# Kernel optimization log

Measured on AMD Instinct MI355X. Metric: run time of the kernel, lower is better.

## Reference

```python
import jax, jax.numpy as jnp
import numpy as np

N_NODES = 100000   # number of graph nodes
N_EDGES = 1600000  # adjacency nnz (avg degree 16)
FEAT_NNZ = 1600000 # sparse feature nnz (~16 per node)
F_IN = 512
F_OUT = 128


def setup_inputs() -> dict:
    key = jax.random.key(0)
    k1, k2, k3, k4, k5, k6 = jax.random.split(key, 6)
    adj_indices = jax.random.randint(k1, (2, N_EDGES), 0, N_NODES, dtype=jnp.int64 if jax.config.jax_enable_x64 else jnp.int32)
    adj_values = jax.random.uniform(k2, (N_EDGES,), dtype=jnp.float32)
    feat_rows = jax.random.randint(k3, (FEAT_NNZ,), 0, N_NODES)
    feat_cols = jax.random.randint(k4, (FEAT_NNZ,), 0, F_IN)
    feat_values = jax.random.uniform(k5, (FEAT_NNZ,), dtype=jnp.float32)
    # xavier_uniform init of the dense weight, as in the torch module
    bound = float(np.sqrt(6.0 / (F_IN + F_OUT)))
    weight = jax.random.uniform(k6, (F_IN, F_OUT), dtype=jnp.float32, minval=-bound, maxval=bound)
    return {
        "adj_indices": adj_indices,
        "adj_values": adj_values,
        "feat_rows": feat_rows,
        "feat_cols": feat_cols,
        "feat_values": feat_values,
        "weight": weight,
        "num_nodes": N_NODES,
    }


def _spmm(rows, cols, vals, num_rows, dense):
    """COO sparse [num_rows, ?] @ dense [?, K] -> [num_rows, K]."""
    msgs = vals[:, None] * dense[cols]          # [nnz, K] gather + scale
    return jax.ops.segment_sum(msgs, rows, num_segments=num_rows)


def reference(adj_indices, adj_values, feat_rows, feat_cols, feat_values, weight, num_nodes):
    # spmm(features, W): sparse [N, F_in] @ [F_in, F_out]
    base_features = _spmm(feat_rows, feat_cols, feat_values, num_nodes, weight)
    # spmm(A_hat, base): sparse [N, N] @ [N, F_out]  -- neighbor aggregation
    out = _spmm(adj_indices[0], adj_indices[1], adj_values, num_nodes, base_features)
    return out
```

## Files before the change

kernel.cpp:

```cpp
#include <hip/hip_runtime.h>
#include <stdint.h>

#define N_NODES 100000
#define F_IN    512
#define F_OUT   128
#define BROWS   128
#define NBKT    ((N_NODES + BROWS - 1) / BROWS)
#define CAP     2560
#define EPB     2048
#define WPAD    136

typedef unsigned short     u16;
typedef unsigned int       u32;
typedef unsigned long long u64;
typedef long long          i64;

__device__ __forceinline__ float b2f(u16 u) {
    union { u32 i; float f; } x; x.i = ((u32)u) << 16; return x.f;
}
__device__ __forceinline__ u16 f2b(float f) {
    u32 i = __float_as_uint(f);
    return (u16)((i + 0x7fffu + ((i >> 16) & 1u)) >> 16);
}
__device__ __forceinline__ float blo(u32 u) { return __uint_as_float(u << 16); }
__device__ __forceinline__ float bhi(u32 u) { return __uint_as_float(u & 0xFFFF0000u); }
__device__ __forceinline__ int ld_idx(const void* p, int i, int w64) {
    return w64 ? (int)((const i64*)p)[i] : ((const int*)p)[i];
}
__device__ __forceinline__ u16 ld_val_bf(const void* p, int i, int f32) {
    return f32 ? f2b(((const float*)p)[i]) : ((const u16*)p)[i];
}

__device__ __forceinline__ void ld_idx4(int* r, const void* p, int g, int w64) {
    if (w64) {
        const i64* q = (const i64*)p + 4 * (size_t)g;
        longlong2 a = *(const longlong2*)q;
        longlong2 b = *(const longlong2*)(q + 2);
        r[0] = (int)a.x; r[1] = (int)a.y; r[2] = (int)b.x; r[3] = (int)b.y;
    } else {
        int4 a = *(const int4*)((const int*)p + 4 * (size_t)g);
        r[0] = a.x; r[1] = a.y; r[2] = a.z; r[3] = a.w;
    }
}
__device__ __forceinline__ void ld_val4(u32* v, const void* p, int g, int f32) {
    if (f32) {
        float4 a = *(const float4*)((const float*)p + 4 * (size_t)g);
        v[0] = f2b(a.x); v[1] = f2b(a.y); v[2] = f2b(a.z); v[3] = f2b(a.w);
    } else {
        ushort4 a = *(const ushort4*)((const u16*)p + 4 * (size_t)g);
        v[0] = a.x; v[1] = a.y; v[2] = a.z; v[3] = a.w;
    }
}

__global__ void sniff_k(const u16* __restrict__ w, const u32* __restrict__ adj,
                        const u32* __restrict__ frows, int* __restrict__ flags,
                        int* __restrict__ gcurF, int* __restrict__ gcurA) {
    int t = threadIdx.x;
    if (t < 64) {
        u32 e0 = (w[t]      >> 7) & 0xFF;
        u32 e1 = (w[64 + t] >> 7) & 0xFF;
        u64 bad = __ballot((e0 > 0x7B) || (e1 > 0x7B));
        u64 za = __ballot(adj[2 * t + 1] == 0u);
        u64 zf = __ballot(frows[2 * t + 1] == 0u);
        if (t == 0) {
            flags[0] = (bad != 0);
            flags[1] = (__popcll(za) >= 32);
            flags[2] = (__popcll(zf) >= 32);
        }
    }
    for (int i = t; i < NBKT; i += 256) { gcurF[i] = 0; gcurA[i] = 0; }
}

__global__ __launch_bounds__(512, 4) void binFA_k(
        const void* __restrict__ frows, const void* __restrict__ fcols,
        const void* __restrict__ fvals, int M, int nFb,
        const void* __restrict__ adjbase, const void* __restrict__ avals, int E,
        const int* __restrict__ flags, int* __restrict__ gcurF, int* __restrict__ gcurA,
        u32* __restrict__ fbkt, u64* __restrict__ abkt) {
    __shared__ int hist[NBKT];
    __shared__ int hbase[NBKT];
    int t = threadIdx.x;
    for (int i = t; i < NBKT; i += 512) hist[i] = 0;
    __syncthreads();
    int f32 = flags[0];
    if ((int)blockIdx.x < nFb) {
        int f64 = flags[2];
        int start = blockIdx.x * EPB;
        int end = min(start + EPB, M);
        int g = (start >> 2) + t;
        int e0 = 4 * g;
        int r[4] = {-1, -1, -1, -1};
        int c[4]; u32 v[4];
        if (e0 + 3 < end) {
            ld_idx4(r, frows, g, f64);
            ld_idx4(c, fcols, g, f64);
            ld_val4(v, fvals, g, f32);
        } else {
            #pragma unroll
            for (int j = 0; j < 4; ++j) if (e0 + j < end) {
                r[j] = ld_idx(frows, e0 + j, f64);
                c[j] = ld_idx(fcols, e0 + j, f64);
                v[j] = ld_val_bf(fvals, e0 + j, f32);
            }
        }
        #pragma unroll
        for (int j = 0; j < 4; ++j) if (r[j] >= 0) atomicAdd(&hist[r[j] >> 7], 1);
        __syncthreads();
        for (int i = t; i < NBKT; i += 512) {
            int h = hist[i];
            hbase[i] = h ? atomicAdd(&gcurF[i], h) : 0;
            hist[i] = 0;
        }
        __syncthreads();
        #pragma unroll
        for (int j = 0; j < 4; ++j) if (r[j] >= 0) {
            int b = r[j] >> 7;
            int pos = hbase[b] + atomicAdd(&hist[b], 1);
            if (pos < CAP)
                fbkt[(size_t)b * CAP + pos] = (v[j] << 16) | ((u32)(r[j] & 127) << 9) | (u32)c[j];
        }
    } else {
        int a64 = flags[1];
        const void* acols = a64 ? (const void*)((const i64*)adjbase + E)
                                : (const void*)((const int*)adjbase + E);
        int start = ((int)blockIdx.x - nFb) * EPB;
        int end = min(start + EPB, E);
        int g = (start >> 2) + t;
        int e0 = 4 * g;
        int r[4] = {-1, -1, -1, -1};
        int c[4]; u32 v[4];
        if (e0 + 3 < end) {
            ld_idx4(r, adjbase, g, a64);
            ld_idx4(c, acols, g, a64);
            ld_val4(v, avals, g, f32);
        } else {
            #pragma unroll
            for (int j = 0; j < 4; ++j) if (e0 + j < end) {
                r[j] = ld_idx(adjbase, e0 + j, a64);
                c[j] = ld_idx(acols, e0 + j, a64);
                v[j] = ld_val_bf(avals, e0 + j, f32);
            }
        }
        #pragma unroll
        for (int j = 0; j < 4; ++j) if (r[j] >= 0) atomicAdd(&hist[r[j] >> 7], 1);
        __syncthreads();
        for (int i = t; i < NBKT; i += 512) {
            int h = hist[i];
            hbase[i] = h ? atomicAdd(&gcurA[i], h) : 0;
            hist[i] = 0;
        }
        __syncthreads();
        #pragma unroll
        for (int j = 0; j < 4; ++j) if (r[j] >= 0) {
            int b = r[j] >> 7;
            int pos = hbase[b] + atomicAdd(&hist[b], 1);
            if (pos < CAP)
                abkt[(size_t)b * CAP + pos] =
                    ((u64)v[j] << 24) | ((u64)(r[j] & 127) << 17) | (u64)(u32)c[j];
        }
    }
}

__global__ __launch_bounds__(512, 1) void stage1_k(const int* __restrict__ cnt,
        const u32* __restrict__ bkts, const void* __restrict__ W,
        const int* __restrict__ flags, u16* __restrict__ base) {
    __shared__ u16 Wlds[F_IN * WPAD];
    __shared__ u32 csr[CAP];
    __shared__ int hcnt[BROWS];
    __shared__ int roff[BROWS + 1];
    __shared__ int cur[BROWS];
    int t = threadIdx.x;
    int f32 = flags[0];
    if (!f32) {
        const u16* Wb = (const u16*)W;
        for (int idx = t; idx < F_IN * 16; idx += 512) {
            int r = idx >> 4, c = idx & 15;
            uint4 q = *(const uint4*)(Wb + r * F_OUT + c * 8);
            *(uint4*)&Wlds[r * WPAD + c * 8] = q;
        }
    }
    int w = t >> 6, lane = t & 63, g16 = lane >> 4, l16 = lane & 15;
    for (int b = blockIdx.x; b < NBKT; b += gridDim.x) {
        int n = cnt[b]; if (n > CAP) n = CAP;
        const u32* ed = bkts + (size_t)b * CAP;
        if (t < BROWS) hcnt[t] = 0;
        __syncthreads();
        u32 pb[5];
        #pragma unroll
        for (int k = 0; k < 5; ++k) { int i = t + k * 512; pb[k] = (i < n) ? ed[i] : 0u; }
        #pragma unroll
        for (int k = 0; k < 5; ++k) { int i = t + k * 512; if (i < n) atomicAdd(&hcnt[(pb[k] >> 9) & 127], 1); }
        __syncthreads();
        if (t < 64) {
            int h0 = hcnt[2 * t], h1 = hcnt[2 * t + 1];
            int s = h0 + h1, v2 = s;
            #pragma unroll
            for (int off = 1; off < 64; off <<= 1) {
                int u = __shfl_up(v2, off);
                if (t >= off) v2 += u;
            }
            int excl = v2 - s;
            roff[2 * t] = excl;     roff[2 * t + 1] = excl + h0;
            cur[2 * t]  = excl;     cur[2 * t + 1]  = excl + h0;
            if (t == 63) roff[128] = v2;
        }
        __syncthreads();
        #pragma unroll
        for (int k = 0; k < 5; ++k) {
            int i = t + k * 512;
            if (i < n) {
                u32 p = pb[k];
                int pos = atomicAdd(&cur[(p >> 9) & 127], 1);
                csr[pos] = p;
            }
        }
        __syncthreads();
        #pragma unroll
        for (int set = 0; set < 4; ++set) {
            int row = set * 32 + w * 4 + g16;
            int s = roff[row], e = roff[row + 1];
            float a0 = 0.f, a1 = 0.f, a2 = 0.f, a3 = 0.f, a4 = 0.f, a5 = 0.f, a6 = 0.f, a7 = 0.f;
            if (f32) {
                const float* Wf = (const float*)W;
                for (int j0 = s; j0 < e; j0 += 4) {
                    u32 p[4]; float4 qa[4], qb[4];
                    #pragma unroll
                    for (int k = 0; k < 4; ++k) { int jk = j0 + k; p[k] = csr[jk < e ? jk : e - 1]; }
                    #pragma unroll
                    for (int k = 0; k < 4; ++k) {
                        const float* wp = Wf + (size_t)(p[k] & 0x1FF) * F_OUT + l16 * 8;
                        qa[k] = *(const float4*)wp;
                        qb[k] = *(const float4*)(wp + 4);
                    }
                    #pragma unroll
                    for (int k = 0; k < 4; ++k) {
                        float v = (j0 + k < e) ? b2f((u16)(p[k] >> 16)) : 0.f;
                        a0 += v * qa[k].x; a1 += v * qa[k].y;
                        a2 += v * qa[k].z; a3 += v * qa[k].w;
                        a4 += v * qb[k].x; a5 += v * qb[k].y;
                        a6 += v * qb[k].z; a7 += v * qb[k].w;
                    }
                }
            } else {
                for (int j0 = s; j0 < e; j0 += 4) {
                    u32 p[4]; uint4 q[4];
                    #pragma unroll
                    for (int k = 0; k < 4; ++k) { int jk = j0 + k; p[k] = csr[jk < e ? jk : e - 1]; }
                    #pragma unroll
                    for (int k = 0; k < 4; ++k)
                        q[k] = *(const uint4*)&Wlds[(p[k] & 0x1FF) * WPAD + l16 * 8];
                    #pragma unroll
                    for (int k = 0; k < 4; ++k) {
                        float v = (j0 + k < e) ? b2f((u16)(p[k] >> 16)) : 0.f;
                        a0 += v * blo(q[k].x); a1 += v * bhi(q[k].x);
                        a2 += v * blo(q[k].y); a3 += v * bhi(q[k].y);
                        a4 += v * blo(q[k].z); a5 += v * bhi(q[k].z);
                        a6 += v * blo(q[k].w); a7 += v * bhi(q[k].w);
                    }
                }
            }
            int gr = b * BROWS + row;
            if (gr < N_NODES) {
                uint4 o;
                o.x = (u32)f2b(a0) | ((u32)f2b(a1) << 16);
                o.y = (u32)f2b(a2) | ((u32)f2b(a3) << 16);
                o.z = (u32)f2b(a4) | ((u32)f2b(a5) << 16);
                o.w = (u32)f2b(a6) | ((u32)f2b(a7) << 16);
                *(uint4*)(base + (size_t)gr * F_OUT + l16 * 8) = o;
            }
        }
        __syncthreads();
    }
}

__global__ __launch_bounds__(512, 4) void stage2_k(const int* __restrict__ cnt,
        const u64* __restrict__ bkts, const u16* __restrict__ base,
        const int* __restrict__ flags, void* __restrict__ out) {
    __shared__ u64 csr[CAP];
    __shared__ int hcnt[BROWS];
    __shared__ int roff[BROWS + 1];
    __shared__ int cur[BROWS];
    int t = threadIdx.x;
    int b = blockIdx.x;
    int n = cnt[b]; if (n > CAP) n = CAP;
    const u64* ed = bkts + (size_t)b * CAP;
    if (t < BROWS) hcnt[t] = 0;
    __syncthreads();
    u64 pb[5];
    #pragma unroll
    for (int k = 0; k < 5; ++k) { int i = t + k * 512; pb[k] = (i < n) ? ed[i] : 0ull; }
    #pragma unroll
    for (int k = 0; k < 5; ++k) { int i = t + k * 512; if (i < n) atomicAdd(&hcnt[(int)((pb[k] >> 17) & 127)], 1); }
    __syncthreads();
    if (t < 64) {
        int h0 = hcnt[2 * t], h1 = hcnt[2 * t + 1];
        int s = h0 + h1, v2 = s;
        #pragma unroll
        for (int off = 1; off < 64; off <<= 1) {
            int u = __shfl_up(v2, off);
            if (t >= off) v2 += u;
        }
        int excl = v2 - s;
        roff[2 * t] = excl;     roff[2 * t + 1] = excl + h0;
        cur[2 * t]  = excl;     cur[2 * t + 1]  = excl + h0;
        if (t == 63) roff[128] = v2;
    }
    __syncthreads();
    #pragma unroll
    for (int k = 0; k < 5; ++k) {
        int i = t + k * 512;
        if (i < n) {
            u64 p = pb[k];
            int pos = atomicAdd(&cur[(int)((p >> 17) & 127)], 1);
            csr[pos] = p;
        }
    }
    __syncthreads();
    int wave = t >> 6, lane = t & 63, g16 = lane >> 4, l16 = lane & 15;
    int f32o = flags[0];
    #pragma unroll
    for (int set = 0; set < 4; ++set) {
        int row = set * 32 + wave * 4 + g16;
        int s = roff[row], e = roff[row + 1];
        float a0 = 0.f, a1 = 0.f, a2 = 0.f, a3 = 0.f, a4 = 0.f, a5 = 0.f, a6 = 0.f, a7 = 0.f;
        for (int j0 = s; j0 < e; j0 += 8) {
            u64 p[8]; uint4 q[8];
            #pragma unroll
            for (int k = 0; k < 8; ++k) { int jk = j0 + k; p[k] = csr[jk < e ? jk : e - 1]; }
            #pragma unroll
            for (int k = 0; k < 8; ++k)
                q[k] = *(const uint4*)(base + (size_t)(u32)(p[k] & 0x1FFFF) * F_OUT + l16 * 8);
            #pragma unroll
            for (int k = 0; k < 8; ++k) {
                float v = (j0 + k < e) ? b2f((u16)(p[k] >> 24)) : 0.f;
                a0 += v * blo(q[k].x); a1 += v * bhi(q[k].x);
                a2 += v * blo(q[k].y); a3 += v * bhi(q[k].y);
                a4 += v * blo(q[k].z); a5 += v * bhi(q[k].z);
                a6 += v * blo(q[k].w); a7 += v * bhi(q[k].w);
            }
        }
        int gr = b * BROWS + row;
        if (gr < N_NODES) {
            if (f32o) {
                float* op = (float*)out + (size_t)gr * F_OUT + l16 * 8;
                float4 o0, o1;
                o0.x = a0; o0.y = a1; o0.z = a2; o0.w = a3;
                o1.x = a4; o1.y = a5; o1.z = a6; o1.w = a7;
                *(float4*)op = o0;
                *(float4*)(op + 4) = o1;
            } else {
                uint4 o;
                o.x = (u32)f2b(a0) | ((u32)f2b(a1) << 16);
                o.y = (u32)f2b(a2) | ((u32)f2b(a3) << 16);
                o.z = (u32)f2b(a4) | ((u32)f2b(a5) << 16);
                o.w = (u32)f2b(a6) | ((u32)f2b(a7) << 16);
                *(uint4*)((u16*)out + (size_t)gr * F_OUT + l16 * 8) = o;
            }
        }
    }
}

extern "C" void kernel_launch(void* const* d_in, const int* in_sizes, int n_in,
                              void* d_out, int out_size, void* d_ws, size_t ws_size,
                              hipStream_t stream) {
    const void* adj_idx   = d_in[0];
    const void* adj_vals  = d_in[1];
    const void* feat_rows = d_in[2];
    const void* feat_cols = d_in[3];
    const void* feat_vals = d_in[4];
    const void* weight    = d_in[5];

    const int E = in_sizes[0] / 2;
    const int M = in_sizes[2];

    char* ws = (char*)d_ws;
    size_t o = 0;
    auto alloc = [&](size_t b) { size_t r = o; o += (b + 255) & ~(size_t)255; return r; };
    int* gcurF = (int*)(ws + alloc((size_t)NBKT * 4));
    int* gcurA = (int*)(ws + alloc((size_t)NBKT * 4));
    int* flags = (int*)(ws + alloc(4 * 4));
    u32* fbkt  = (u32*)(ws + alloc((size_t)NBKT * CAP * 4));
    u64* abkt  = (u64*)(ws + alloc((size_t)NBKT * CAP * 8));
    u16* base  = (u16*)(ws + alloc((size_t)N_NODES * F_OUT * 2));
    (void)ws_size;

    const int nFb = (M + EPB - 1) / EPB;
    const int nAb = (E + EPB - 1) / EPB;

    sniff_k<<<1, 256, 0, stream>>>((const u16*)weight, (const u32*)adj_idx,
                                   (const u32*)feat_rows, flags, gcurF, gcurA);
    binFA_k<<<nFb + nAb, 512, 0, stream>>>(feat_rows, feat_cols, feat_vals, M, nFb,
                                           adj_idx, adj_vals, E,
                                           flags, gcurF, gcurA, fbkt, abkt);
    stage1_k<<<256, 512, 0, stream>>>(gcurF, fbkt, weight, flags, base);
    stage2_k<<<NBKT, 512, 0, stream>>>(gcurA, abkt, base, flags, d_out);
}
```

Measured before the change: 254.0 us.

## Fold dtype sniffing into kernels, memset counters, double-buffer stage2 gathers

Removes the separate sniff kernel: every kernel now recomputes the dtype/width flags into shared memory itself, and the bucket counters are zeroed with an async memset. The binning kernel moves to 1024 threads and 4096 edges per block. Stage2 gets a software-pipelined gather that prefetches the next four base rows while accumulating the current four, with higher occupancy launch bounds. Risks include extra per-block redundant sniff loads, a leftover dead binFA_k stub, and stage2 reading sf without a sync right after sniff3.

New measurement: 246.1 us. -3.1%, faster.

```diff
diff --git a/kernel.cpp b/kernel.cpp
--- a/kernel.cpp
+++ b/kernel.cpp
@@ -7,7 +7,7 @@
 #define BROWS   128
 #define NBKT    ((N_NODES + BROWS - 1) / BROWS)
 #define CAP     2560
-#define EPB     2048
+#define EPB     4096
 #define WPAD    136
 
 typedef unsigned short     u16;
@@ -52,10 +52,8 @@
     }
 }
 
-__global__ void sniff_k(const u16* __restrict__ w, const u32* __restrict__ adj,
-                        const u32* __restrict__ frows, int* __restrict__ flags,
-                        int* __restrict__ gcurF, int* __restrict__ gcurA) {
-    int t = threadIdx.x;
+__device__ __forceinline__ void sniff3(const u16* w, const u32* adj, const u32* frows,
+                                       int* sf, int t) {
     if (t < 64) {
         u32 e0 = (w[t]      >> 7) & 0xFF;
         u32 e1 = (w[64 + t] >> 7) & 0xFF;
@@ -63,28 +61,44 @@
         u64 za = __ballot(adj[2 * t + 1] == 0u);
         u64 zf = __ballot(frows[2 * t + 1] == 0u);
         if (t == 0) {
-            flags[0] = (bad != 0);
-            flags[1] = (__popcll(za) >= 32);
-            flags[2] = (__popcll(zf) >= 32);
-        }
-    }
-    for (int i = t; i < NBKT; i += 256) { gcurF[i] = 0; gcurA[i] = 0; }
-}
-
-__global__ __launch_bounds__(512, 4) void binFA_k(
+            sf[0] = (bad != 0);
+            sf[1] = (__popcll(za) >= 32);
+            sf[2] = (__popcll(zf) >= 32);
+        }
+    }
+}
+
+__global__ __launch_bounds__(1024, 8) void binFA_k(
         const void* __restrict__ frows, const void* __restrict__ fcols,
         const void* __restrict__ fvals, int M, int nFb,
         const void* __restrict__ adjbase, const void* __restrict__ avals, int E,
-        const int* __restrict__ flags, int* __restrict__ gcurF, int* __restrict__ gcurA,
+        int* __restrict__ gcurF, int* __restrict__ gcurA,
         u32* __restrict__ fbkt, u64* __restrict__ abkt) {
     __shared__ int hist[NBKT];
     __shared__ int hbase[NBKT];
+    __shared__ int sf[3];
     int t = threadIdx.x;
-    for (int i = t; i < NBKT; i += 512) hist[i] = 0;
-    __syncthreads();
-    int f32 = flags[0];
+    sniff3((const u16*)fvals == nullptr ? nullptr : (const u16*)0, nullptr, nullptr, sf, 1024);
+    (void)sf;
+}
+
+__global__ __launch_bounds__(1024, 8) void binFA2_k(
+        const void* __restrict__ frows, const void* __restrict__ fcols,
+        const void* __restrict__ fvals, int M, int nFb,
+        const void* __restrict__ adjbase, const void* __restrict__ avals, int E,
+        const u16* __restrict__ weight,
+        int* __restrict__ gcurF, int* __restrict__ gcurA,
+        u32* __restrict__ fbkt, u64* __restrict__ abkt) {
+    __shared__ int hist[NBKT];
+    __shared__ int hbase[NBKT];
+    __shared__ int sf[3];
+    int t = threadIdx.x;
+    sniff3(weight, (const u32*)adjbase, (const u32*)frows, sf, t);
+    for (int i = t; i < NBKT; i += 1024) hist[i] = 0;
+    __syncthreads();
+    int f32 = sf[0];
     if ((int)blockIdx.x < nFb) {
-        int f64 = flags[2];
+        int f64 = sf[2];
         int start = blockIdx.x * EPB;
         int end = min(start + EPB, M);
         int g = (start >> 2) + t;
@@ -106,7 +120,7 @@
         #pragma unroll
         for (int j = 0; j < 4; ++j) if (r[j] >= 0) atomicAdd(&hist[r[j] >> 7], 1);
         __syncthreads();
-        for (int i = t; i < NBKT; i += 512) {
+        for (int i = t; i < NBKT; i += 1024) {
             int h = hist[i];
             hbase[i] = h ? atomicAdd(&gcurF[i], h) : 0;
             hist[i] = 0;
@@ -120,7 +134,7 @@
                 fbkt[(size_t)b * CAP + pos] = (v[j] << 16) | ((u32)(r[j] & 127) << 9) | (u32)c[j];
         }
     } else {
-        int a64 = flags[1];
+        int a64 = sf[1];
         const void* acols = a64 ? (const void*)((const i64*)adjbase + E)
                                 : (const void*)((const int*)adjbase + E);
         int start = ((int)blockIdx.x - nFb) * EPB;
@@ -144,7 +158,7 @@
         #pragma unroll
         for (int j = 0; j < 4; ++j) if (r[j] >= 0) atomicAdd(&hist[r[j] >> 7], 1);
         __syncthreads();
-        for (int i = t; i < NBKT; i += 512) {
+        for (int i = t; i < NBKT; i += 1024) {
             int h = hist[i];
             hbase[i] = h ? atomicAdd(&gcurA[i], h) : 0;
             hist[i] = 0;
@@ -163,14 +177,18 @@
 
 __global__ __launch_bounds__(512, 1) void stage1_k(const int* __restrict__ cnt,
         const u32* __restrict__ bkts, const void* __restrict__ W,
-        const int* __restrict__ flags, u16* __restrict__ base) {
+        const u32* __restrict__ adjsn, const u32* __restrict__ frsn,
+        u16* __restrict__ base) {
     __shared__ u16 Wlds[F_IN * WPAD];
     __shared__ u32 csr[CAP];
     __shared__ int hcnt[BROWS];
     __shared__ int roff[BROWS + 1];
     __shared__ int cur[BROWS];
+    __shared__ int sf[3];
     int t = threadIdx.x;
-    int f32 = flags[0];
+    sniff3((const u16*)W, adjsn, frsn, sf, t);
+    __syncthreads();
+    int f32 = sf[0];
     if (!f32) {
         const u16* Wb = (const u16*)W;
         for (int idx = t; idx < F_IN * 16; idx += 512) {
@@ -273,14 +291,23 @@
     }
 }
 
-__global__ __launch_bounds__(512, 4) void stage2_k(const int* __restrict__ cnt,
+#define S2ACC(Q) do { \
+    a0 += v * blo((Q).x); a1 += v * bhi((Q).x); \
+    a2 += v * blo((Q).y); a3 += v * bhi((Q).y); \
+    a4 += v * blo((Q).z); a5 += v * bhi((Q).z); \
+    a6 += v * blo((Q).w); a7 += v * bhi((Q).w); } while (0)
+
+__global__ __launch_bounds__(512, 8) void stage2_k(const int* __restrict__ cnt,
         const u64* __restrict__ bkts, const u16* __restrict__ base,
-        const int* __restrict__ flags, void* __restrict__ out) {
+        const void* __restrict__ W, const u32* __restrict__ adjsn,
+        const u32* __restrict__ frsn, void* __restrict__ out) {
     __shared__ u64 csr[CAP];
     __shared__ int hcnt[BROWS];
     __shared__ int roff[BROWS + 1];
     __shared__ int cur[BROWS];
+    __shared__ int sf[3];
     int t = threadIdx.x;
+    sniff3((const u16*)W, adjsn, frsn, sf, t);
     int b = blockIdx.x;
     int n = cnt[b]; if (n > CAP) n = CAP;
     const u64* ed = bkts + (size_t)b * CAP;
@@ -317,26 +344,44 @@
     }
     __syncthreads();
     int wave = t >> 6, lane = t & 63, g16 = lane >> 4, l16 = lane & 15;
-    int f32o = flags[0];
+    int f32o = sf[0];
     #pragma unroll
     for (int set = 0; set < 4; ++set) {
         int row = set * 32 + wave * 4 + g16;
         int s = roff[row], e = roff[row + 1];
         float a0 = 0.f, a1 = 0.f, a2 = 0.f, a3 = 0.f, a4 = 0.f, a5 = 0.f, a6 = 0.f, a7 = 0.f;
-        for (int j0 = s; j0 < e; j0 += 8) {
-            u64 p[8]; uint4 q[8];
-            #pragma unroll
-            for (int k = 0; k < 8; ++k) { int jk = j0 + k; p[k] = csr[jk < e ? jk : e - 1]; }
-            #pragma unroll
-            for (int k = 0; k < 8; ++k)
-                q[k] = *(const uint4*)(base + (size_t)(u32)(p[k] & 0x1FFFF) * F_OUT + l16 * 8);
-            #pragma unroll
-            for (int k = 0; k < 8; ++k) {
-                float v = (j0 + k < e) ? b2f((u16)(p[k] >> 24)) : 0.f;
-                a0 += v * blo(q[k].x); a1 += v * bhi(q[k].x);
-                a2 += v * blo(q[k].y); a3 += v * bhi(q[k].y);
-                a4 += v * blo(q[k].z); a5 += v * bhi(q[k].z);
-                a6 += v * blo(q[k].w); a7 += v * bhi(q[k].w);
+        if (s < e) {
+            int fb = s;
+            uint4 qc0, qc1, qc2, qc3;
+            {
+                u64 p0 = csr[s];
+                u64 p1 = csr[s + 1 < e ? s + 1 : fb];
+                u64 p2 = csr[s + 2 < e ? s + 2 : fb];
+                u64 p3 = csr[s + 3 < e ? s + 3 : fb];
+                qc0 = *(const uint4*)(base + (size_t)(u32)(p0 & 0x1FFFF) * F_OUT + l16 * 8);
+                qc1 = *(const uint4*)(base + (size_t)(u32)(p1 & 0x1FFFF) * F_OUT + l16 * 8);
+                qc2 = *(const uint4*)(base + (size_t)(u32)(p2 & 0x1FFFF) * F_OUT + l16 * 8);
+                qc3 = *(const uint4*)(base + (size_t)(u32)(p3 & 0x1FFFF) * F_OUT + l16 * 8);
+            }
+            for (int j0 = s; j0 < e; j0 += 4) {
+                int j1 = j0 + 4;
+                uint4 qn0, qn1, qn2, qn3;
+                {
+                    u64 p0 = csr[j1     < e ? j1     : fb];
+                    u64 p1 = csr[j1 + 1 < e ? j1 + 1 : fb];
+                    u64 p2 = csr[j1 + 2 < e ? j1 + 2 : fb];
+                    u64 p3 = csr[j1 + 3 < e ? j1 + 3 : fb];
+                    qn0 = *(const uint4*)(base + (size_t)(u32)(p0 & 0x1FFFF) * F_OUT + l16 * 8);
+                    qn1 = *(const uint4*)(base + (size_t)(u32)(p1 & 0x1FFFF) * F_OUT + l16 * 8);
+                    qn2 = *(const uint4*)(base + (size_t)(u32)(p2 & 0x1FFFF) * F_OUT + l16 * 8);
+                    qn3 = *(const uint4*)(base + (size_t)(u32)(p3 & 0x1FFFF) * F_OUT + l16 * 8);
+                }
+                float v;
+                v = b2f((u16)(csr[j0] >> 24));                                    S2ACC(qc0);
+                v = (j0 + 1 < e) ? b2f((u16)(csr[j0 + 1] >> 24)) : 0.f;           S2ACC(qc1);
+                v = (j0 + 2 < e) ? b2f((u16)(csr[j0 + 2] >> 24)) : 0.f;           S2ACC(qc2);
+                v = (j0 + 3 < e) ? b2f((u16)(csr[j0 + 3] >> 24)) : 0.f;           S2ACC(qc3);
+                qc0 = qn0; qc1 = qn1; qc2 = qn2; qc3 = qn3;
             }
         }
         int gr = b * BROWS + row;
@@ -378,7 +423,7 @@
     auto alloc = [&](size_t b) { size_t r = o; o += (b + 255) & ~(size_t)255; return r; };
     int* gcurF = (int*)(ws + alloc((size_t)NBKT * 4));
     int* gcurA = (int*)(ws + alloc((size_t)NBKT * 4));
-    int* flags = (int*)(ws + alloc(4 * 4));
+    size_t cur_end = o;
     u32* fbkt  = (u32*)(ws + alloc((size_t)NBKT * CAP * 4));
     u64* abkt  = (u64*)(ws + alloc((size_t)NBKT * CAP * 8));
     u16* base  = (u16*)(ws + alloc((size_t)N_NODES * F_OUT * 2));
@@ -387,11 +432,12 @@
     const int nFb = (M + EPB - 1) / EPB;
     const int nAb = (E + EPB - 1) / EPB;
 
-    sniff_k<<<1, 256, 0, stream>>>((const u16*)weight, (const u32*)adj_idx,
-                                   (const u32*)feat_rows, flags, gcurF, gcurA);
-    binFA_k<<<nFb + nAb, 512, 0, stream>>>(feat_rows, feat_cols, feat_vals, M, nFb,
-                                           adj_idx, adj_vals, E,
-                                           flags, gcurF, gcurA, fbkt, abkt);
-    stage1_k<<<256, 512, 0, stream>>>(gcurF, fbkt, weight, flags, base);
-    stage2_k<<<NBKT, 512, 0, stream>>>(gcurA, abkt, base, flags, d_out);
-}
+    hipMemsetAsync(ws, 0, cur_end, stream);
+    binFA2_k<<<nFb + nAb, 1024, 0, stream>>>(feat_rows, feat_cols, feat_vals, M, nFb,
+                                             adj_idx, adj_vals, E, (const u16*)weight,
+                                             gcurF, gcurA, fbkt, abkt);
+    stage1_k<<<256, 512, 0, stream>>>(gcurF, fbkt, weight,
+                                      (const u32*)adj_idx, (const u32*)feat_rows, base);
+    stage2_k<<<NBKT, 512, 0, stream>>>(gcurA, abkt, base, weight,
+                                       (const u32*)adj_idx, (const u32*)feat_rows, d_out);
+}
```
